# Kernel tuning notes

Hardware: AMD Instinct MI355X
Metric: run time of the kernel (lower is better)

Reference implementation:

```python
import jax, jax.numpy as jnp
import numpy as np

N_SENTS, N_ENTS, BATCH, DIM, HEADS = 64, 16, 64, 512, 8


def setup_inputs() -> dict:
    key = jax.random.key(0)
    ks = jax.random.split(key, 10)
    se = N_SENTS * N_ENTS
    s = 0.02  # init scale for projection weights
    entities = jax.random.normal(ks[0], (se, BATCH, DIM), dtype=jnp.float32)
    query_param = jax.random.uniform(ks[1], (1, 1, DIM), jnp.float32, -1.0, 1.0)
    wq = jax.random.normal(ks[2], (DIM, DIM), jnp.float32) * s
    wk = jax.random.normal(ks[3], (DIM, DIM), jnp.float32) * s
    wv = jax.random.normal(ks[4], (DIM, DIM), jnp.float32) * s
    wo = jax.random.normal(ks[5], (DIM, DIM), jnp.float32) * s
    bq = jax.random.normal(ks[6], (DIM,), jnp.float32) * s
    bk = jax.random.normal(ks[7], (DIM,), jnp.float32) * s
    bv = jax.random.normal(ks[8], (DIM,), jnp.float32) * s
    bo = jax.random.normal(ks[9], (DIM,), jnp.float32) * s
    return {"entities": entities, "query_param": query_param,
            "wq": wq, "wk": wk, "wv": wv, "wo": wo,
            "bq": bq, "bk": bk, "bv": bv, "bo": bo,
            "n_sents": N_SENTS}


def reference(entities, query_param, wq, wk, wv, wo, bq, bk, bv, bo, n_sents):
    # entities: [n_sents*n_ents, batch, dim]
    se, b, d = entities.shape
    n_ents = se // n_sents
    h = HEADS
    hd = d // h

    # Learned single query broadcast to every (sentence, batch) slot.
    q_in = jnp.broadcast_to(query_param, (n_sents, b, d))
    q = q_in @ wq.T + bq            # [n_sents, b, d]
    k = entities @ wk.T + bk        # [se, b, d]
    v = entities @ wv.T + bv        # [se, b, d]

    # Split heads -> [b, h, len, hd]
    qh = q.reshape(n_sents, b, h, hd).transpose(1, 2, 0, 3)
    kh = k.reshape(se, b, h, hd).transpose(1, 2, 0, 3)
    vh = v.reshape(se, b, h, hd).transpose(1, 2, 0, 3)

    scale = jnp.asarray(1.0 / np.sqrt(hd), dtype=qh.dtype)
    scores = jnp.einsum('bhqd,bhkd->bhqk', qh, kh) * scale  # [b,h,n_sents,se]

    # Block-diagonal mask: query i attends only to keys [i*n_ents, (i+1)*n_ents)
    valid = (jnp.arange(se) // n_ents)[None, :] == jnp.arange(n_sents)[:, None]
    scores = jnp.where(valid[None, None], scores, jnp.finfo(scores.dtype).min)

    attn = jax.nn.softmax(scores, axis=-1)
    ctx = jnp.einsum('bhqk,bhkd->bhqd', attn, vh)            # [b,h,n_sents,hd]
    out = ctx.transpose(2, 0, 1, 3).reshape(n_sents, b, d)   # merge heads
    return out @ wo.T + bo                                   # [n_sents, b, d]
```

## Files before the change

kernel.cpp:

```cpp
#include <hip/hip_runtime.h>
#include <stdint.h>

#define HEADS 8
#define DIM   512
#define HD    64
#define NE    16
#define NS    64
#define NB    64

typedef short bf16x8 __attribute__((ext_vector_type(8)));
typedef float f32x4  __attribute__((ext_vector_type(4)));

__device__ __forceinline__ unsigned short f2bf(float f) {
    union { float f; uint32_t u; } v; v.f = f;
    uint32_t u = v.u;
    u += 0x7fffu + ((u >> 16) & 1u);
    return (unsigned short)(u >> 16);
}
__device__ __forceinline__ float bf_lo(uint32_t u) {
    union { uint32_t u; float f; } v; v.u = u << 16; return v.f;
}
__device__ __forceinline__ float bf_hi(uint32_t u) {
    union { uint32_t u; float f; } v; v.u = u & 0xffff0000u; return v.f;
}

__device__ __forceinline__ uint32_t cvt2(float a, float b) {
    uint32_t r;
    asm("v_cvt_pk_bf16_f32 %0, %1, %2" : "=v"(r) : "v"(a), "v"(b));
    return r;
}
__device__ __forceinline__ uint2 cvt4(float4 v) {
    return (uint2){cvt2(v.x, v.y), cvt2(v.z, v.w)};
}
__device__ __forceinline__ uint2 cvt4f(f32x4 v) {
    return (uint2){cvt2(v.x, v.y), cvt2(v.z, v.w)};
}

__global__ __launch_bounds__(256) void k_prep(
    const float* __restrict__ qp, const float* __restrict__ wq,
    const float* __restrict__ bq, const float* __restrict__ wk,
    const float* __restrict__ wv, const float* __restrict__ wo,
    unsigned short* __restrict__ u_bf,
    unsigned short* __restrict__ wv_bf, unsigned short* __restrict__ wo_bf)
{
    const int bid = blockIdx.x;
    const int t = threadIdx.x;
    if (bid < 16) {
        const int h = bid >> 1, ch = bid & 1;
        __shared__ float qs[HD];
        {
            const int j = t >> 2, q = t & 3;
            const float* w = wq + (size_t)(h * HD + j) * DIM + q * 128;
            const float* qq = qp + q * 128;
            float a = 0.f;
            #pragma unroll 8
            for (int i = 0; i < 128; i++) a += w[i] * qq[i];
            a += __shfl_xor(a, 1);
            a += __shfl_xor(a, 2);
            if (q == 0) qs[j] = a + bq[h * HD + j];
        }
        __syncthreads();
        const int c = ch * 256 + t;
        const float* w = wk + (size_t)(h * HD) * DIM + c;
        float acc = 0.f;
        #pragma unroll 8
        for (int j = 0; j < HD; j++) acc += qs[j] * w[(size_t)j * DIM];
        u_bf[h * DIM + c] = f2bf(acc);
        u_bf[(h + 8) * DIM + c] = 0;
        return;
    }
    const bool is_v = bid < 272;
    const float* src = is_v ? wv : wo;
    unsigned short* dst = is_v ? wv_bf : wo_bf;
    const int li = ((is_v ? bid - 16 : bid - 272) * 1024 + t * 4);
    const float4 v = *(const float4*)(src + li);
    ushort4 hv;
    hv.x = f2bf(v.x); hv.y = f2bf(v.y); hv.z = f2bf(v.z); hv.w = f2bf(v.w);
    *(ushort4*)(dst + li) = hv;
}

__global__ __launch_bounds__(256, 4) void k_attn(
    const float* __restrict__ ents, const unsigned short* __restrict__ u_bf,
    unsigned short* __restrict__ weighted)
{
    __shared__ unsigned short ent[2 * NE * DIM];
    __shared__ float attn_s[2][NE][8];
    const int t = threadIdx.x;
    const int bid = blockIdx.x;
    const int s = bid >> 5;
    const int bg = (bid & 31) << 1;
    const int w = t >> 6, lane = t & 63;

    {
        const int bb = t >> 7, d4 = t & 127;
        const float* p = ents + ((size_t)((s * NE) * NB + bg + bb) << 9) + (d4 << 2);
        const uint32_t dstb = (uint32_t)(t << 3);
        #pragma unroll
        for (int i = 0; i < NE; i++) {
            const float4 v = *(const float4*)(p + (size_t)i * (NB * DIM));
            const uint2 hv = cvt4(v);
            const uint32_t off = ((uint32_t)(i << 11) | dstb) ^ (uint32_t)((i & 7) << 4);
            *(uint2*)((char*)ent + off) = hv;
        }
    }
    __syncthreads();

    if (w < 2) {
        const int m = lane & 15, g = lane >> 4;
        const uint32_t swz = (uint32_t)((m & 7) << 4);
        const uint32_t rowb = (uint32_t)((m * 2 + w) << 10);
        const unsigned short* urow = u_bf + m * DIM + g * 8;
        f32x4 acc = {0.f, 0.f, 0.f, 0.f};
        #pragma unroll
        for (int ks = 0; ks < 16; ks++) {
            const int kp = g * 8 + ks * 32;
            const bf16x8 af = *(const bf16x8*)((const char*)ent + ((rowb + (uint32_t)(kp << 1)) ^ swz));
            const bf16x8 bf = *(const bf16x8*)(urow + ks * 32);
            acc = __builtin_amdgcn_mfma_f32_16x16x32_bf16(af, bf, acc, 0, 0, 0);
        }
        const float scale = 0.125f;
        float s0 = acc[0]*scale, s1 = acc[1]*scale, s2 = acc[2]*scale, s3 = acc[3]*scale;
        float mx = fmaxf(fmaxf(s0, s1), fmaxf(s2, s3));
        mx = fmaxf(mx, __shfl_xor(mx, 16));
        mx = fmaxf(mx, __shfl_xor(mx, 32));
        const float p0 = __expf(s0 - mx), p1 = __expf(s1 - mx);
        const float p2 = __expf(s2 - mx), p3 = __expf(s3 - mx);
        float sm = p0 + p1 + p2 + p3;
        sm += __shfl_xor(sm, 16);
        sm += __shfl_xor(sm, 32);
        const float inv = 1.f / sm;
        if (m < HEADS) {
            attn_s[w][4 * g + 0][m] = p0 * inv;
            attn_s[w][4 * g + 1][m] = p1 * inv;
            attn_s[w][4 * g + 2][m] = p2 * inv;
            attn_s[w][4 * g + 3][m] = p3 * inv;
        }
    }
    __syncthreads();

    {
        const int bb = w & 1, dh = w >> 1;
        const uint32_t dbyte = (uint32_t)((dh << 9) | (lane << 3));
        f32x4 acc[HEADS];
        #pragma unroll
        for (int h = 0; h < HEADS; h++) acc[h] = (f32x4){0.f, 0.f, 0.f, 0.f};

        #pragma unroll
        for (int e = 0; e < NE; e++) {
            const uint32_t off = ((uint32_t)((e * 2 + bb) << 10) | dbyte) ^ (uint32_t)((e & 7) << 4);
            const uint2 rv = *(const uint2*)((const char*)ent + off);
            const f32x4 ev = {bf_lo(rv.x), bf_hi(rv.x), bf_lo(rv.y), bf_hi(rv.y)};
            const f32x4 a0 = *(const f32x4*)&attn_s[bb][e][0];
            const f32x4 a1 = *(const f32x4*)&attn_s[bb][e][4];
            acc[0] += a0.x * ev; acc[1] += a0.y * ev;
            acc[2] += a0.z * ev; acc[3] += a0.w * ev;
            acc[4] += a1.x * ev; acc[5] += a1.y * ev;
            acc[6] += a1.z * ev; acc[7] += a1.w * ev;
        }
        const int sb = s * NB + bg + bb;
        const int d0 = (dh << 8) | (lane << 2);
        unsigned short* wrow = weighted + ((size_t)sb << 12) + d0;
        #pragma unroll
        for (int h = 0; h < HEADS; h++) {
            *(uint2*)(wrow + h * DIM) = cvt4f(acc[h]);
        }
    }
}

template <typename CT>
__global__ __launch_bounds__(256) void k_gemm(
    const unsigned short* __restrict__ A, int lda, int aOffY,
    const unsigned short* __restrict__ B, int ldb, int bOffY,
    const float* __restrict__ bias, CT* __restrict__ C, int ldc, int cOffY, int K)
{
    __shared__ unsigned short a_s[64][72];
    __shared__ unsigned short b_s[64][72];
    const int t = threadIdx.x;
    const int m0 = blockIdx.x * 64;
    const int y  = blockIdx.y;
    const int w = t >> 6, l = t & 63;
    const int m = l & 15, g = l >> 4;
    const int lr = t >> 2, lk = (t & 3) * 16;

    const unsigned short* Ap = A + (size_t)(m0 + lr) * lda + (size_t)aOffY * y;
    const unsigned short* Bp = B + (size_t)(bOffY * y + lr) * ldb;

    f32x4 acc[4];
    #pragma unroll
    for (int i = 0; i < 4; i++) acc[i] = (f32x4){0.f, 0.f, 0.f, 0.f};

    for (int k0 = 0; k0 < K; k0 += 64) {
        const ushort4 av0 = *(const ushort4*)(Ap + k0 + lk);
        const ushort4 av1 = *(const ushort4*)(Ap + k0 + lk + 4);
        const ushort4 av2 = *(const ushort4*)(Ap + k0 + lk + 8);
        const ushort4 av3 = *(const ushort4*)(Ap + k0 + lk + 12);
        const ushort4 bv0 = *(const ushort4*)(Bp + k0 + lk);
        const ushort4 bv1 = *(const ushort4*)(Bp + k0 + lk + 4);
        const ushort4 bv2 = *(const ushort4*)(Bp + k0 + lk + 8);
        const ushort4 bv3 = *(const ushort4*)(Bp + k0 + lk + 12);
        *(ushort4*)&a_s[lr][lk]      = av0;
        *(ushort4*)&a_s[lr][lk + 4]  = av1;
        *(ushort4*)&a_s[lr][lk + 8]  = av2;
        *(ushort4*)&a_s[lr][lk + 12] = av3;
        *(ushort4*)&b_s[lr][lk]      = bv0;
        *(ushort4*)&b_s[lr][lk + 4]  = bv1;
        *(ushort4*)&b_s[lr][lk + 8]  = bv2;
        *(ushort4*)&b_s[lr][lk + 12] = bv3;
        __syncthreads();
        #pragma unroll
        for (int kk = 0; kk < 64; kk += 32) {
            const int kp = kk + g * 8;
            const bf16x8 af = *(const bf16x8*)&a_s[w * 16 + m][kp];
            const bf16x8 b0 = *(const bf16x8*)&b_s[ 0 + m][kp];
            const bf16x8 b1 = *(const bf16x8*)&b_s[16 + m][kp];
            const bf16x8 b2 = *(const bf16x8*)&b_s[32 + m][kp];
            const bf16x8 b3 = *(const bf16x8*)&b_s[48 + m][kp];
            acc[0] = __builtin_amdgcn_mfma_f32_16x16x32_bf16(af, b0, acc[0], 0, 0, 0);
            acc[1] = __builtin_amdgcn_mfma_f32_16x16x32_bf16(af, b1, acc[1], 0, 0, 0);
            acc[2] = __builtin_amdgcn_mfma_f32_16x16x32_bf16(af, b2, acc[2], 0, 0, 0);
            acc[3] = __builtin_amdgcn_mfma_f32_16x16x32_bf16(af, b3, acc[3], 0, 0, 0);
        }
        __syncthreads();
    }

    const int colbase = cOffY * y;
    #pragma unroll
    for (int nt = 0; nt < 4; nt++) {
        const int col = colbase + nt * 16 + m;
        const float bs = bias[col];
        #pragma unroll
        for (int j = 0; j < 4; j++) {
            const int row = m0 + w * 16 + g * 4 + j;
            const float val = acc[nt][j] + bs;
            if (sizeof(CT) == 2) {
                ((unsigned short*)C)[(size_t)row * ldc + col] = f2bf(val);
            } else {
                ((float*)C)[(size_t)row * ldc + col] = val;
            }
        }
    }
}

extern "C" void kernel_launch(void* const* d_in, const int* in_sizes, int n_in,
                              void* d_out, int out_size, void* d_ws, size_t ws_size,
                              hipStream_t stream)
{
    const float* ents = (const float*)d_in[0];
    const float* qp   = (const float*)d_in[1];
    const float* wq   = (const float*)d_in[2];
    const float* wk   = (const float*)d_in[3];
    const float* wv   = (const float*)d_in[4];
    const float* wo   = (const float*)d_in[5];
    const float* bq   = (const float*)d_in[6];
    const float* bv   = (const float*)d_in[8];
    const float* bo   = (const float*)d_in[9];

    char* ws = (char*)d_ws;
    unsigned short* u_bf     = (unsigned short*)ws;
    unsigned short* wv_bf    = (unsigned short*)(ws + 65536);
    unsigned short* wo_bf    = (unsigned short*)(ws + 65536 + 524288);
    unsigned short* weighted = (unsigned short*)(ws + 2097152);
    unsigned short* ctx      = (unsigned short*)(ws + 2097152 + 33554432);

    k_prep <<<528, 256, 0, stream>>>(qp, wq, bq, wk, wv, wo, u_bf, wv_bf, wo_bf);
    k_attn <<<2048, 256, 0, stream>>>(ents, u_bf, weighted);
    k_gemm<unsigned short><<<dim3(64, 8), 256, 0, stream>>>(
        weighted, HEADS * DIM, DIM, wv_bf, DIM, HD, bv, ctx, DIM, HD, DIM);
    k_gemm<float><<<dim3(64, 8), 256, 0, stream>>>(
        ctx, DIM, 0, wo_bf, DIM, HD, bo, (float*)d_out, DIM, HD, DIM);
}
```

Measured before the change: 65.19 us.

## Fuse weight bf16 conversion into GEMMs, keep entities in registers, prefetch tiles

Drops the separate conversion of wv/wo to bf16 in k_prep. The GEMM now reads fp32 weights and converts them while staging into shared memory, and it prefetches the next K tile into registers during the MFMA loop. In k_attn the fp32 entity vectors stay in registers for the weighted-sum phase instead of being re-read from bf16 shared memory, and the occupancy hint drops from 4 to 3 to fit the extra registers. The weighted sum now uses full fp32 entities. Risks include higher register pressure and twice the weight bytes read by every GEMM block.

New measurement: 69.58 us. +6.7%, slower.

```diff
diff --git a/kernel.cpp b/kernel.cpp
--- a/kernel.cpp
+++ b/kernel.cpp
@@ -17,12 +17,6 @@
     u += 0x7fffu + ((u >> 16) & 1u);
     return (unsigned short)(u >> 16);
 }
-__device__ __forceinline__ float bf_lo(uint32_t u) {
-    union { uint32_t u; float f; } v; v.u = u << 16; return v.f;
-}
-__device__ __forceinline__ float bf_hi(uint32_t u) {
-    union { uint32_t u; float f; } v; v.u = u & 0xffff0000u; return v.f;
-}
 
 __device__ __forceinline__ uint32_t cvt2(float a, float b) {
     uint32_t r;
@@ -39,47 +33,34 @@
 __global__ __launch_bounds__(256) void k_prep(
     const float* __restrict__ qp, const float* __restrict__ wq,
     const float* __restrict__ bq, const float* __restrict__ wk,
-    const float* __restrict__ wv, const float* __restrict__ wo,
-    unsigned short* __restrict__ u_bf,
-    unsigned short* __restrict__ wv_bf, unsigned short* __restrict__ wo_bf)
+    unsigned short* __restrict__ u_bf)
 {
     const int bid = blockIdx.x;
     const int t = threadIdx.x;
-    if (bid < 16) {
-        const int h = bid >> 1, ch = bid & 1;
-        __shared__ float qs[HD];
-        {
-            const int j = t >> 2, q = t & 3;
-            const float* w = wq + (size_t)(h * HD + j) * DIM + q * 128;
-            const float* qq = qp + q * 128;
-            float a = 0.f;
-            #pragma unroll 8
-            for (int i = 0; i < 128; i++) a += w[i] * qq[i];
-            a += __shfl_xor(a, 1);
-            a += __shfl_xor(a, 2);
-            if (q == 0) qs[j] = a + bq[h * HD + j];
-        }
-        __syncthreads();
-        const int c = ch * 256 + t;
-        const float* w = wk + (size_t)(h * HD) * DIM + c;
-        float acc = 0.f;
+    const int h = bid >> 1, ch = bid & 1;
+    __shared__ float qs[HD];
+    {
+        const int j = t >> 2, q = t & 3;
+        const float* w = wq + (size_t)(h * HD + j) * DIM + q * 128;
+        const float* qq = qp + q * 128;
+        float a = 0.f;
         #pragma unroll 8
-        for (int j = 0; j < HD; j++) acc += qs[j] * w[(size_t)j * DIM];
-        u_bf[h * DIM + c] = f2bf(acc);
-        u_bf[(h + 8) * DIM + c] = 0;
-        return;
-    }
-    const bool is_v = bid < 272;
-    const float* src = is_v ? wv : wo;
-    unsigned short* dst = is_v ? wv_bf : wo_bf;
-    const int li = ((is_v ? bid - 16 : bid - 272) * 1024 + t * 4);
-    const float4 v = *(const float4*)(src + li);
-    ushort4 hv;
-    hv.x = f2bf(v.x); hv.y = f2bf(v.y); hv.z = f2bf(v.z); hv.w = f2bf(v.w);
-    *(ushort4*)(dst + li) = hv;
-}
-
-__global__ __launch_bounds__(256, 4) void k_attn(
+        for (int i = 0; i < 128; i++) a += w[i] * qq[i];
+        a += __shfl_xor(a, 1);
+        a += __shfl_xor(a, 2);
+        if (q == 0) qs[j] = a + bq[h * HD + j];
+    }
+    __syncthreads();
+    const int c = ch * 256 + t;
+    const float* w = wk + (size_t)(h * HD) * DIM + c;
+    float acc = 0.f;
+    #pragma unroll 8
+    for (int j = 0; j < HD; j++) acc += qs[j] * w[(size_t)j * DIM];
+    u_bf[h * DIM + c] = f2bf(acc);
+    u_bf[(h + 8) * DIM + c] = 0;
+}
+
+__global__ __launch_bounds__(256, 3) void k_attn(
     const float* __restrict__ ents, const unsigned short* __restrict__ u_bf,
     unsigned short* __restrict__ weighted)
 {
@@ -90,16 +71,19 @@
     const int s = bid >> 5;
     const int bg = (bid & 31) << 1;
     const int w = t >> 6, lane = t & 63;
-
+    const int bb = t >> 7, d4 = t & 127;
+
+    const float* p = ents + ((size_t)((s * NE) * NB + bg + bb) << 9) + (d4 << 2);
+    float4 v[NE];
+    #pragma unroll
+    for (int e = 0; e < NE; e++)
+        v[e] = *(const float4*)(p + (size_t)e * (NB * DIM));
     {
-        const int bb = t >> 7, d4 = t & 127;
-        const float* p = ents + ((size_t)((s * NE) * NB + bg + bb) << 9) + (d4 << 2);
         const uint32_t dstb = (uint32_t)(t << 3);
         #pragma unroll
-        for (int i = 0; i < NE; i++) {
-            const float4 v = *(const float4*)(p + (size_t)i * (NB * DIM));
-            const uint2 hv = cvt4(v);
-            const uint32_t off = ((uint32_t)(i << 11) | dstb) ^ (uint32_t)((i & 7) << 4);
+        for (int e = 0; e < NE; e++) {
+            const uint2 hv = cvt4(v[e]);
+            const uint32_t off = ((uint32_t)(e << 11) | dstb) ^ (uint32_t)((e & 7) << 4);
             *(uint2*)((char*)ent + off) = hv;
         }
     }
@@ -139,17 +123,13 @@
     __syncthreads();
 
     {
-        const int bb = w & 1, dh = w >> 1;
-        const uint32_t dbyte = (uint32_t)((dh << 9) | (lane << 3));
         f32x4 acc[HEADS];
         #pragma unroll
         for (int h = 0; h < HEADS; h++) acc[h] = (f32x4){0.f, 0.f, 0.f, 0.f};
 
         #pragma unroll
         for (int e = 0; e < NE; e++) {
-            const uint32_t off = ((uint32_t)((e * 2 + bb) << 10) | dbyte) ^ (uint32_t)((e & 7) << 4);
-            const uint2 rv = *(const uint2*)((const char*)ent + off);
-            const f32x4 ev = {bf_lo(rv.x), bf_hi(rv.x), bf_lo(rv.y), bf_hi(rv.y)};
+            const f32x4 ev = {v[e].x, v[e].y, v[e].z, v[e].w};
             const f32x4 a0 = *(const f32x4*)&attn_s[bb][e][0];
             const f32x4 a1 = *(const f32x4*)&attn_s[bb][e][4];
             acc[0] += a0.x * ev; acc[1] += a0.y * ev;
@@ -158,8 +138,7 @@
             acc[6] += a1.z * ev; acc[7] += a1.w * ev;
         }
         const int sb = s * NB + bg + bb;
-        const int d0 = (dh << 8) | (lane << 2);
-        unsigned short* wrow = weighted + ((size_t)sb << 12) + d0;
+        unsigned short* wrow = weighted + ((size_t)sb << 12) + (d4 << 2);
         #pragma unroll
         for (int h = 0; h < HEADS; h++) {
             *(uint2*)(wrow + h * DIM) = cvt4f(acc[h]);
@@ -170,7 +149,7 @@
 template <typename CT>
 __global__ __launch_bounds__(256) void k_gemm(
     const unsigned short* __restrict__ A, int lda, int aOffY,
-    const unsigned short* __restrict__ B, int ldb, int bOffY,
+    const float* __restrict__ B, int ldb, int bOffY,
     const float* __restrict__ bias, CT* __restrict__ C, int ldc, int cOffY, int K)
 {
     __shared__ unsigned short a_s[64][72];
@@ -182,31 +161,36 @@
     const int m = l & 15, g = l >> 4;
     const int lr = t >> 2, lk = (t & 3) * 16;
 
-    const unsigned short* Ap = A + (size_t)(m0 + lr) * lda + (size_t)aOffY * y;
-    const unsigned short* Bp = B + (size_t)(bOffY * y + lr) * ldb;
+    const unsigned short* Ap = A + (size_t)(m0 + lr) * lda + (size_t)aOffY * y + lk;
+    const float* Bp = B + (size_t)(bOffY * y + lr) * ldb + lk;
+
+    ushort4 av[4];
+    float4  bv[4];
+    #pragma unroll
+    for (int i = 0; i < 4; i++) {
+        av[i] = *(const ushort4*)(Ap + 4 * i);
+        bv[i] = *(const float4*)(Bp + 4 * i);
+    }
 
     f32x4 acc[4];
     #pragma unroll
     for (int i = 0; i < 4; i++) acc[i] = (f32x4){0.f, 0.f, 0.f, 0.f};
 
     for (int k0 = 0; k0 < K; k0 += 64) {
-        const ushort4 av0 = *(const ushort4*)(Ap + k0 + lk);
-        const ushort4 av1 = *(const ushort4*)(Ap + k0 + lk + 4);
-        const ushort4 av2 = *(const ushort4*)(Ap + k0 + lk + 8);
-        const ushort4 av3 = *(const ushort4*)(Ap + k0 + lk + 12);
-        const ushort4 bv0 = *(const ushort4*)(Bp + k0 + lk);
-        const ushort4 bv1 = *(const ushort4*)(Bp + k0 + lk + 4);
-        const ushort4 bv2 = *(const ushort4*)(Bp + k0 + lk + 8);
-        const ushort4 bv3 = *(const ushort4*)(Bp + k0 + lk + 12);
-        *(ushort4*)&a_s[lr][lk]      = av0;
-        *(ushort4*)&a_s[lr][lk + 4]  = av1;
-        *(ushort4*)&a_s[lr][lk + 8]  = av2;
-        *(ushort4*)&a_s[lr][lk + 12] = av3;
-        *(ushort4*)&b_s[lr][lk]      = bv0;
-        *(ushort4*)&b_s[lr][lk + 4]  = bv1;
-        *(ushort4*)&b_s[lr][lk + 8]  = bv2;
-        *(ushort4*)&b_s[lr][lk + 12] = bv3;
+        #pragma unroll
+        for (int i = 0; i < 4; i++) {
+            *(ushort4*)&a_s[lr][lk + 4 * i] = av[i];
+            const uint2 h = cvt4(bv[i]);
+            *(uint2*)&b_s[lr][lk + 4 * i] = h;
+        }
         __syncthreads();
+        if (k0 + 64 < K) {
+            #pragma unroll
+            for (int i = 0; i < 4; i++) {
+                av[i] = *(const ushort4*)(Ap + k0 + 64 + 4 * i);
+                bv[i] = *(const float4*)(Bp + k0 + 64 + 4 * i);
+            }
+        }
         #pragma unroll
         for (int kk = 0; kk < 64; kk += 32) {
             const int kp = kk + g * 8;
@@ -257,15 +241,13 @@
 
     char* ws = (char*)d_ws;
     unsigned short* u_bf     = (unsigned short*)ws;
-    unsigned short* wv_bf    = (unsigned short*)(ws + 65536);
-    unsigned short* wo_bf    = (unsigned short*)(ws + 65536 + 524288);
     unsigned short* weighted = (unsigned short*)(ws + 2097152);
     unsigned short* ctx      = (unsigned short*)(ws + 2097152 + 33554432);
 
-    k_prep <<<528, 256, 0, stream>>>(qp, wq, bq, wk, wv, wo, u_bf, wv_bf, wo_bf);
+    k_prep <<<16, 256, 0, stream>>>(qp, wq, bq, wk, u_bf);
     k_attn <<<2048, 256, 0, stream>>>(ents, u_bf, weighted);
     k_gemm<unsigned short><<<dim3(64, 8), 256, 0, stream>>>(
-        weighted, HEADS * DIM, DIM, wv_bf, DIM, HD, bv, ctx, DIM, HD, DIM);
+        weighted, HEADS * DIM, DIM, wv, DIM, HD, bv, ctx, DIM, HD, DIM);
     k_gemm<float><<<dim3(64, 8), 256, 0, stream>>>(
-        ctx, DIM, 0, wo_bf, DIM, HD, bo, (float*)d_out, DIM, HD, DIM);
-}
+        ctx, DIM, 0, wo, DIM, HD, bo, (float*)d_out, DIM, HD, DIM);
+}
```

## Split attention kernel to one (sentence,batch) per block, doubling grid

Applied to the files above, without the earlier changes.

k_attn now handles one (sentence, batch) pair per block instead of two, halving shared memory and launching 4096 blocks with a higher occupancy hint. The load loop, score MFMA (one wave instead of two) and weighted-sum stage are reindexed so each thread covers two dims of all heads. The aim is more blocks resident per CU to hide the global load latency of the entity tile, at the cost of narrower 32-bit LDS and global stores and fewer waves doing the score MFMA per block.

Measured after the change: 62.03 us. -4.9%, faster.

```diff
diff --git a/kernel.cpp b/kernel.cpp
--- a/kernel.cpp
+++ b/kernel.cpp
@@ -30,9 +30,6 @@
     return r;
 }
 __device__ __forceinline__ uint2 cvt4(float4 v) {
-    return (uint2){cvt2(v.x, v.y), cvt2(v.z, v.w)};
-}
-__device__ __forceinline__ uint2 cvt4f(f32x4 v) {
     return (uint2){cvt2(v.x, v.y), cvt2(v.z, v.w)};
 }
 
@@ -79,36 +76,34 @@
     *(ushort4*)(dst + li) = hv;
 }
 
-__global__ __launch_bounds__(256, 4) void k_attn(
+__global__ __launch_bounds__(256, 6) void k_attn(
     const float* __restrict__ ents, const unsigned short* __restrict__ u_bf,
     unsigned short* __restrict__ weighted)
 {
-    __shared__ unsigned short ent[2 * NE * DIM];
-    __shared__ float attn_s[2][NE][8];
+    __shared__ unsigned short ent[NE * DIM];
+    __shared__ float attn_s[NE][8];
     const int t = threadIdx.x;
     const int bid = blockIdx.x;
-    const int s = bid >> 5;
-    const int bg = (bid & 31) << 1;
-    const int w = t >> 6, lane = t & 63;
+    const int s = bid >> 6, b = bid & 63;
 
     {
-        const int bb = t >> 7, d4 = t & 127;
-        const float* p = ents + ((size_t)((s * NE) * NB + bg + bb) << 9) + (d4 << 2);
-        const uint32_t dstb = (uint32_t)(t << 3);
-        #pragma unroll
-        for (int i = 0; i < NE; i++) {
-            const float4 v = *(const float4*)(p + (size_t)i * (NB * DIM));
+        const float* base = ents + ((size_t)(s * NE) * NB + b) * DIM;
+        #pragma unroll
+        for (int i = 0; i < 8; i++) {
+            const int c = t + 256 * i;
+            const int e = c >> 7, d4 = c & 127;
+            const float4 v = *(const float4*)(base + (size_t)e * (NB * DIM) + (d4 << 2));
             const uint2 hv = cvt4(v);
-            const uint32_t off = ((uint32_t)(i << 11) | dstb) ^ (uint32_t)((i & 7) << 4);
+            const uint32_t off = (uint32_t)((e << 10) | (d4 << 3)) ^ (uint32_t)((e & 7) << 4);
             *(uint2*)((char*)ent + off) = hv;
         }
     }
     __syncthreads();
 
-    if (w < 2) {
-        const int m = lane & 15, g = lane >> 4;
+    if (t < 64) {
+        const int m = t & 15, g = t >> 4;
         const uint32_t swz = (uint32_t)((m & 7) << 4);
-        const uint32_t rowb = (uint32_t)((m * 2 + w) << 10);
+        const uint32_t rowb = (uint32_t)(m << 10);
         const unsigned short* urow = u_bf + m * DIM + g * 8;
         f32x4 acc = {0.f, 0.f, 0.f, 0.f};
         #pragma unroll
@@ -130,39 +125,40 @@
         sm += __shfl_xor(sm, 32);
         const float inv = 1.f / sm;
         if (m < HEADS) {
-            attn_s[w][4 * g + 0][m] = p0 * inv;
-            attn_s[w][4 * g + 1][m] = p1 * inv;
-            attn_s[w][4 * g + 2][m] = p2 * inv;
-            attn_s[w][4 * g + 3][m] = p3 * inv;
+            attn_s[4 * g + 0][m] = p0 * inv;
+            attn_s[4 * g + 1][m] = p1 * inv;
+            attn_s[4 * g + 2][m] = p2 * inv;
+            attn_s[4 * g + 3][m] = p3 * inv;
         }
     }
     __syncthreads();
 
     {
-        const int bb = w & 1, dh = w >> 1;
-        const uint32_t dbyte = (uint32_t)((dh << 9) | (lane << 3));
-        f32x4 acc[HEADS];
-        #pragma unroll
-        for (int h = 0; h < HEADS; h++) acc[h] = (f32x4){0.f, 0.f, 0.f, 0.f};
+        const int d0 = t << 1;
+        float accx[HEADS], accy[HEADS];
+        #pragma unroll
+        for (int h = 0; h < HEADS; h++) { accx[h] = 0.f; accy[h] = 0.f; }
 
         #pragma unroll
         for (int e = 0; e < NE; e++) {
-            const uint32_t off = ((uint32_t)((e * 2 + bb) << 10) | dbyte) ^ (uint32_t)((e & 7) << 4);
-            const uint2 rv = *(const uint2*)((const char*)ent + off);
-            const f32x4 ev = {bf_lo(rv.x), bf_hi(rv.x), bf_lo(rv.y), bf_hi(rv.y)};
-            const f32x4 a0 = *(const f32x4*)&attn_s[bb][e][0];
-            const f32x4 a1 = *(const f32x4*)&attn_s[bb][e][4];
-            acc[0] += a0.x * ev; acc[1] += a0.y * ev;
-            acc[2] += a0.z * ev; acc[3] += a0.w * ev;
-            acc[4] += a1.x * ev; acc[5] += a1.y * ev;
-            acc[6] += a1.z * ev; acc[7] += a1.w * ev;
-        }
-        const int sb = s * NB + bg + bb;
-        const int d0 = (dh << 8) | (lane << 2);
-        unsigned short* wrow = weighted + ((size_t)sb << 12) + d0;
+            const uint32_t off = (uint32_t)((e << 10) | (d0 << 1)) ^ (uint32_t)((e & 7) << 4);
+            const uint32_t rv = *(const uint32_t*)((const char*)ent + off);
+            const float ev0 = bf_lo(rv), ev1 = bf_hi(rv);
+            const f32x4 a0 = *(const f32x4*)&attn_s[e][0];
+            const f32x4 a1 = *(const f32x4*)&attn_s[e][4];
+            accx[0] += a0.x * ev0; accy[0] += a0.x * ev1;
+            accx[1] += a0.y * ev0; accy[1] += a0.y * ev1;
+            accx[2] += a0.z * ev0; accy[2] += a0.z * ev1;
+            accx[3] += a0.w * ev0; accy[3] += a0.w * ev1;
+            accx[4] += a1.x * ev0; accy[4] += a1.x * ev1;
+            accx[5] += a1.y * ev0; accy[5] += a1.y * ev1;
+            accx[6] += a1.z * ev0; accy[6] += a1.z * ev1;
+            accx[7] += a1.w * ev0; accy[7] += a1.w * ev1;
+        }
+        unsigned short* wrow = weighted + ((size_t)bid << 12) + d0;
         #pragma unroll
         for (int h = 0; h < HEADS; h++) {
-            *(uint2*)(wrow + h * DIM) = cvt4f(acc[h]);
+            *(uint32_t*)(wrow + h * DIM) = cvt2(accx[h], accy[h]);
         }
     }
 }
@@ -263,7 +259,7 @@
     unsigned short* ctx      = (unsigned short*)(ws + 2097152 + 33554432);
 
     k_prep <<<528, 256, 0, stream>>>(qp, wq, bq, wk, wv, wo, u_bf, wv_bf, wo_bf);
-    k_attn <<<2048, 256, 0, stream>>>(ents, u_bf, weighted);
+    k_attn <<<4096, 256, 0, stream>>>(ents, u_bf, weighted);
     k_gemm<unsigned short><<<dim3(64, 8), 256, 0, stream>>>(
         weighted, HEADS * DIM, DIM, wv_bf, DIM, HD, bv, ctx, DIM, HD, DIM);
     k_gemm<float><<<dim3(64, 8), 256, 0, stream>>>(
```
